# Kernel optimization log

Hardware: AMD Instinct MI355X
Metric: run time of the kernel (lower is better)

## Reference

```python
import jax, jax.numpy as jnp
import numpy as np

N_NODES = 100000
N_EDGES = 600000
N_GRAPHS = 64
DIM_IN = 128


def setup_inputs() -> dict:
    key = jax.random.key(0)
    ks = jax.random.split(key, 12)
    s = 0.05
    return {
        "feat": jax.random.normal(ks[0], (N_NODES, DIM_IN), jnp.float32),
        "Wself1": jax.random.normal(ks[1], (DIM_IN, 100), jnp.float32) * s,
        "Wneigh1": jax.random.normal(ks[2], (DIM_IN, 100), jnp.float32) * s,
        "b1": jnp.zeros((100,), jnp.float32),
        "Wself2": jax.random.normal(ks[3], (100, 20), jnp.float32) * s,
        "Wneigh2": jax.random.normal(ks[4], (100, 20), jnp.float32) * s,
        "b2": jnp.zeros((20,), jnp.float32),
        "fc1_w": jax.random.normal(ks[5], (20, 10), jnp.float32) * s,
        "fc1_b": jnp.zeros((10,), jnp.float32),
        "fc2_w": jax.random.normal(ks[6], (10, 1), jnp.float32) * s,
        "fc2_b": jnp.zeros((1,), jnp.float32),
        "src": jax.random.randint(ks[7], (N_EDGES,), 0, N_NODES, jnp.int32),
        "dst": jax.random.randint(ks[8], (N_EDGES,), 0, N_NODES, jnp.int32),
        "graph_ids": jnp.sort(jax.random.randint(ks[9], (N_NODES,), 0, N_GRAPHS, jnp.int32)),
    }


def _sage_mean(x, src, dst, inv_deg, Wself, Wneigh, b):
    # DGL SAGEConv(aggr='mean'): fc_self(h) + fc_neigh(mean of in-neighbor feats)
    msg = x[src]  # [E, d] gather
    agg = jax.ops.segment_sum(msg, dst, num_segments=N_NODES) * inv_deg  # [N, d]
    return x @ Wself + agg @ Wneigh + b


def reference(feat, Wself1, Wneigh1, b1, Wself2, Wneigh2, b2,
              fc1_w, fc1_b, fc2_w, fc2_b, src, dst, graph_ids):
    ones_e = jnp.ones((src.shape[0],), feat.dtype)
    deg = jax.ops.segment_sum(ones_e, dst, num_segments=N_NODES)
    inv_deg = (1.0 / jnp.maximum(deg, 1.0))[:, None]  # zero in-degree -> agg stays 0

    h = jax.nn.relu(_sage_mean(feat, src, dst, inv_deg, Wself1, Wneigh1, b1))
    h = jax.nn.relu(_sage_mean(h, src, dst, inv_deg, Wself2, Wneigh2, b2))

    # dgl.mean_nodes: per-graph mean over nodes
    ones_n = jnp.ones((h.shape[0],), h.dtype)
    counts = jax.ops.segment_sum(ones_n, graph_ids, num_segments=N_GRAPHS)
    hg = jax.ops.segment_sum(h, graph_ids, num_segments=N_GRAPHS) / jnp.maximum(counts, 1.0)[:, None]

    out = jax.nn.relu(hg @ fc1_w + fc1_b) @ fc2_w + fc2_b  # [G, 1]
    return out
```

## Files before the change

kernel.cpp:

```cpp
#include <hip/hip_runtime.h>
#include <cstddef>

#define N_NODES  100000
#define N_EDGES  600000
#define N_GRAPHS 64

__device__ __forceinline__ void atomAddF(float* p, float v) {
    unsafeAtomicAdd(p, v);
}

__device__ __forceinline__ float f4get(const float4& v, int i) {
    return i == 0 ? v.x : i == 1 ? v.y : i == 2 ? v.z : v.w;
}

typedef __attribute__((address_space(1))) void GV;
typedef __attribute__((address_space(3))) void LV;
__device__ __forceinline__ void gload16(const float* g, float* l) {
    __builtin_amdgcn_global_load_lds((GV*)g, (LV*)l, 16, 0, 0);
}

__global__ __launch_bounds__(256) void deg_count(const int* __restrict__ dst,
                                                 int* __restrict__ deg) {
    int e = blockIdx.x * 256 + threadIdx.x;
    if (e < N_EDGES) atomicAdd(deg + dst[e], 1);
}

__global__ __launch_bounds__(256)
void alloc_ranges(const int* __restrict__ deg, int* __restrict__ beg,
                  int* __restrict__ cur, int* __restrict__ counter) {
    int n = blockIdx.x * 256 + threadIdx.x;
    int d = (n < N_NODES) ? deg[n] : 0;
    int lane = threadIdx.x & 63, wid = threadIdx.x >> 6;
    int incl = d;
#pragma unroll
    for (int o = 1; o < 64; o <<= 1) {
        int v = __shfl_up(incl, o);
        if (lane >= o) incl += v;
    }
    __shared__ int wsum[4];
    __shared__ int blockBase;
    if (lane == 63) wsum[wid] = incl;
    __syncthreads();
    if (threadIdx.x == 0) {
        int tot = wsum[0] + wsum[1] + wsum[2] + wsum[3];
        blockBase = atomicAdd(counter, tot);
    }
    __syncthreads();
    int base = blockBase;
    for (int w = 0; w < wid; ++w) base += wsum[w];
    int start = base + incl - d;
    if (n < N_NODES) { beg[n] = start; cur[n] = start; }
}

__global__ __launch_bounds__(256)
void csr_fill(const int* __restrict__ src, const int* __restrict__ dst,
              int* __restrict__ cur, int* __restrict__ csr_src) {
    int e = blockIdx.x * 256 + threadIdx.x;
    if (e >= N_EDGES) return;
    int p = atomicAdd(cur + dst[e], 1);
    csr_src[p] = src[e];
}

__global__ __launch_bounds__(256, 6)
void gemm1(const float* __restrict__ feat, const float* __restrict__ Wself,
           const float* __restrict__ Wneigh,
           float* __restrict__ S1, float* __restrict__ N1) {
    __shared__ float As[40 * 16];
    __shared__ float Bs[16][200];
    const int tid  = threadIdx.x;
    const int m0   = blockIdx.x * 40;
    const int wave = tid >> 6;
    const int lane = tid & 63;
    const bool active = tid < 250;
    const int tr  = tid / 25;
    const int tcc = tid % 25;
    const int sw  = tr & 3;

    float4 acc0[4], acc1[4];
#pragma unroll
    for (int i = 0; i < 4; ++i) {
        acc0[i] = make_float4(0.f, 0.f, 0.f, 0.f);
        acc1[i] = make_float4(0.f, 0.f, 0.f, 0.f);
    }

    for (int kt = 0; kt < 8; ++kt) {
        const int k0 = kt * 16;
        if (kt) __syncthreads();

        if (lane < 40) {
            int u  = wave * 40 + lane;
            int r  = u >> 2;
            int k4 = (u & 3) ^ ((r >> 2) & 3);
            gload16(feat + (size_t)(m0 + r) * 128 + k0 + k4 * 4, &As[wave * 160]);
        }
        for (int idx = tid; idx < 800; idx += 256) {
            int k = idx / 50, n4 = idx % 50;
            int n = n4 * 4;
            int gk = k0 + k;
            float4 v;
            if (n < 100) v = *reinterpret_cast<const float4*>(Wself + gk * 100 + n);
            else         v = *reinterpret_cast<const float4*>(Wneigh + gk * 100 + (n - 100));
            *reinterpret_cast<float4*>(&Bs[k][n]) = v;
        }
        __syncthreads();

        if (active) {
            const int abase = tr * 64;
#pragma unroll
            for (int g = 0; g < 4; ++g) {
                const int ac = ((g ^ sw) << 2);
                const float4 a0 = *reinterpret_cast<const float4*>(&As[abase +  0 + ac]);
                const float4 a1 = *reinterpret_cast<const float4*>(&As[abase + 16 + ac]);
                const float4 a2 = *reinterpret_cast<const float4*>(&As[abase + 32 + ac]);
                const float4 a3 = *reinterpret_cast<const float4*>(&As[abase + 48 + ac]);
#pragma unroll
                for (int kl = 0; kl < 4; ++kl) {
                    const int k = g * 4 + kl;
                    const float4 b0 = *reinterpret_cast<const float4*>(&Bs[k][tcc * 4]);
                    const float4 b1 = *reinterpret_cast<const float4*>(&Bs[k][100 + tcc * 4]);
                    const float v0 = f4get(a0, kl), v1 = f4get(a1, kl);
                    const float v2 = f4get(a2, kl), v3 = f4get(a3, kl);
                    acc0[0].x = fmaf(v0, b0.x, acc0[0].x); acc0[0].y = fmaf(v0, b0.y, acc0[0].y);
                    acc0[0].z = fmaf(v0, b0.z, acc0[0].z); acc0[0].w = fmaf(v0, b0.w, acc0[0].w);
                    acc1[0].x = fmaf(v0, b1.x, acc1[0].x); acc1[0].y = fmaf(v0, b1.y, acc1[0].y);
                    acc1[0].z = fmaf(v0, b1.z, acc1[0].z); acc1[0].w = fmaf(v0, b1.w, acc1[0].w);
                    acc0[1].x = fmaf(v1, b0.x, acc0[1].x); acc0[1].y = fmaf(v1, b0.y, acc0[1].y);
                    acc0[1].z = fmaf(v1, b0.z, acc0[1].z); acc0[1].w = fmaf(v1, b0.w, acc0[1].w);
                    acc1[1].x = fmaf(v1, b1.x, acc1[1].x); acc1[1].y = fmaf(v1, b1.y, acc1[1].y);
                    acc1[1].z = fmaf(v1, b1.z, acc1[1].z); acc1[1].w = fmaf(v1, b1.w, acc1[1].w);
                    acc0[2].x = fmaf(v2, b0.x, acc0[2].x); acc0[2].y = fmaf(v2, b0.y, acc0[2].y);
                    acc0[2].z = fmaf(v2, b0.z, acc0[2].z); acc0[2].w = fmaf(v2, b0.w, acc0[2].w);
                    acc1[2].x = fmaf(v2, b1.x, acc1[2].x); acc1[2].y = fmaf(v2, b1.y, acc1[2].y);
                    acc1[2].z = fmaf(v2, b1.z, acc1[2].z); acc1[2].w = fmaf(v2, b1.w, acc1[2].w);
                    acc0[3].x = fmaf(v3, b0.x, acc0[3].x); acc0[3].y = fmaf(v3, b0.y, acc0[3].y);
                    acc0[3].z = fmaf(v3, b0.z, acc0[3].z); acc0[3].w = fmaf(v3, b0.w, acc0[3].w);
                    acc1[3].x = fmaf(v3, b1.x, acc1[3].x); acc1[3].y = fmaf(v3, b1.y, acc1[3].y);
                    acc1[3].z = fmaf(v3, b1.z, acc1[3].z); acc1[3].w = fmaf(v3, b1.w, acc1[3].w);
                }
            }
        }
    }

    if (active) {
        const int c = tcc * 4;
#pragma unroll
        for (int i = 0; i < 4; ++i) {
            int gr = m0 + tr * 4 + i;
            *reinterpret_cast<float4*>(S1 + (size_t)gr * 100 + c) = acc0[i];
            *reinterpret_cast<float4*>(N1 + (size_t)gr * 100 + c) = acc1[i];
        }
    }
}

__global__ __launch_bounds__(256)
void aggregate1(const float* __restrict__ N1, const float* __restrict__ S1,
                const float* __restrict__ b1, const int* __restrict__ csr_src,
                const int* __restrict__ beg, const int* __restrict__ cur,
                float* __restrict__ h1) {
    int n  = blockIdx.x * 8 + (threadIdx.x >> 5);
    int c4 = threadIdx.x & 31;
    if (n >= N_NODES || c4 >= 25) return;
    int b = beg[n], end = cur[n];
    float4 acc = make_float4(0.f, 0.f, 0.f, 0.f);
    int j = b;
    for (; j + 1 < end; j += 2) {
        int s0 = csr_src[j], s1 = csr_src[j + 1];
        float4 v0 = *reinterpret_cast<const float4*>(N1 + (size_t)s0 * 100 + c4 * 4);
        float4 v1 = *reinterpret_cast<const float4*>(N1 + (size_t)s1 * 100 + c4 * 4);
        acc.x += v0.x + v1.x; acc.y += v0.y + v1.y;
        acc.z += v0.z + v1.z; acc.w += v0.w + v1.w;
    }
    if (j < end) {
        int s = csr_src[j];
        float4 v = *reinterpret_cast<const float4*>(N1 + (size_t)s * 100 + c4 * 4);
        acc.x += v.x; acc.y += v.y; acc.z += v.z; acc.w += v.w;
    }
    float inv = 1.0f / (float)max(end - b, 1);
    float4 s  = *reinterpret_cast<const float4*>(S1 + (size_t)n * 100 + c4 * 4);
    float4 bb = *reinterpret_cast<const float4*>(b1 + c4 * 4);
    float4 h;
    h.x = fmaxf(fmaf(acc.x, inv, s.x) + bb.x, 0.f);
    h.y = fmaxf(fmaf(acc.y, inv, s.y) + bb.y, 0.f);
    h.z = fmaxf(fmaf(acc.z, inv, s.z) + bb.z, 0.f);
    h.w = fmaxf(fmaf(acc.w, inv, s.w) + bb.w, 0.f);
    *reinterpret_cast<float4*>(h1 + (size_t)n * 100 + c4 * 4) = h;
}

__global__ __launch_bounds__(256)
void gemm2(const float* __restrict__ h1,
           const float* __restrict__ Ws2, const float* __restrict__ Wn2,
           float* __restrict__ S2, float* __restrict__ N2) {
    __shared__ float As[64 * 100];
    __shared__ float Bs[100][40];
    const int tid  = threadIdx.x;
    const int m0   = blockIdx.x * 64;
    const int wave = tid >> 6;
    const int lane = tid & 63;

#pragma unroll
    for (int t = 0; t < 7; ++t) {
        int u0 = t * 256 + wave * 64;
        if (u0 < 1600) {
            int u  = u0 + lane;
            int r  = u / 25, c4 = u % 25;
            int gr = m0 + r; if (gr >= N_NODES) gr = N_NODES - 1;
            gload16(h1 + (size_t)gr * 100 + c4 * 4, &As[u0 * 4]);
        }
    }
    for (int idx = tid; idx < 1000; idx += 256) {
        int k = idx / 10, n4 = idx % 10;
        int n = n4 * 4;
        float4 v;
        if (n < 20) v = *reinterpret_cast<const float4*>(Ws2 + k * 20 + n);
        else        v = *reinterpret_cast<const float4*>(Wn2 + k * 20 + (n - 20));
        *reinterpret_cast<float4*>(&Bs[k][n]) = v;
    }
    __syncthreads();

    const int tr = tid >> 4, tc = tid & 15;
    if (tc < 10) {
        float acc[4][4] = {};
#pragma unroll 4
        for (int k = 0; k < 100; ++k) {
            float a0 = As[(tr * 4 + 0) * 100 + k];
            float a1 = As[(tr * 4 + 1) * 100 + k];
            float a2 = As[(tr * 4 + 2) * 100 + k];
            float a3 = As[(tr * 4 + 3) * 100 + k];
            float4 b = *reinterpret_cast<const float4*>(&Bs[k][tc * 4]);
            acc[0][0] += a0 * b.x; acc[0][1] += a0 * b.y; acc[0][2] += a0 * b.z; acc[0][3] += a0 * b.w;
            acc[1][0] += a1 * b.x; acc[1][1] += a1 * b.y; acc[1][2] += a1 * b.z; acc[1][3] += a1 * b.w;
            acc[2][0] += a2 * b.x; acc[2][1] += a2 * b.y; acc[2][2] += a2 * b.z; acc[2][3] += a2 * b.w;
            acc[3][0] += a3 * b.x; acc[3][1] += a3 * b.y; acc[3][2] += a3 * b.z; acc[3][3] += a3 * b.w;
        }
#pragma unroll
        for (int i = 0; i < 4; ++i) {
            int gr = m0 + tr * 4 + i;
            if (gr >= N_NODES) continue;
            int n = tc * 4;
            float4 v = make_float4(acc[i][0], acc[i][1], acc[i][2], acc[i][3]);
            if (n < 20) *reinterpret_cast<float4*>(S2 + (size_t)gr * 20 + n) = v;
            else        *reinterpret_cast<float4*>(N2 + (size_t)gr * 20 + (n - 20)) = v;
        }
    }
}

__global__ __launch_bounds__(256)
void aggregate2(const float* __restrict__ N2, const float* __restrict__ S2,
                const float* __restrict__ b2, const int* __restrict__ csr_src,
                const int* __restrict__ beg, const int* __restrict__ cur,
                float* __restrict__ h2) {
    int n  = blockIdx.x * 32 + (threadIdx.x >> 3);
    int c4 = threadIdx.x & 7;
    if (n >= N_NODES || c4 >= 5) return;
    int b = beg[n], end = cur[n];
    float4 acc = make_float4(0.f, 0.f, 0.f, 0.f);
    int j = b;
    for (; j + 1 < end; j += 2) {
        int s0 = csr_src[j], s1 = csr_src[j + 1];
        float4 v0 = *reinterpret_cast<const float4*>(N2 + (size_t)s0 * 20 + c4 * 4);
        float4 v1 = *reinterpret_cast<const float4*>(N2 + (size_t)s1 * 20 + c4 * 4);
        acc.x += v0.x + v1.x; acc.y += v0.y + v1.y;
        acc.z += v0.z + v1.z; acc.w += v0.w + v1.w;
    }
    if (j < end) {
        int s = csr_src[j];
        float4 v = *reinterpret_cast<const float4*>(N2 + (size_t)s * 20 + c4 * 4);
        acc.x += v.x; acc.y += v.y; acc.z += v.z; acc.w += v.w;
    }
    float inv = 1.0f / (float)max(end - b, 1);
    float4 s  = *reinterpret_cast<const float4*>(S2 + (size_t)n * 20 + c4 * 4);
    float4 bb = *reinterpret_cast<const float4*>(b2 + c4 * 4);
    float4 h;
    h.x = fmaxf(fmaf(acc.x, inv, s.x) + bb.x, 0.f);
    h.y = fmaxf(fmaf(acc.y, inv, s.y) + bb.y, 0.f);
    h.z = fmaxf(fmaf(acc.z, inv, s.z) + bb.z, 0.f);
    h.w = fmaxf(fmaf(acc.w, inv, s.w) + bb.w, 0.f);
    *reinterpret_cast<float4*>(h2 + (size_t)n * 20 + c4 * 4) = h;
}

__global__ __launch_bounds__(256)
void pool_kernel(const float* __restrict__ h2, const int* __restrict__ gids,
                 float* __restrict__ pool, float* __restrict__ cnt) {
    int n = blockIdx.x * 256 + threadIdx.x;
    float h[20];
    int g = -1;
    if (n < N_NODES) {
        g = gids[n];
#pragma unroll
        for (int q = 0; q < 5; ++q) {
            float4 v = *reinterpret_cast<const float4*>(h2 + (size_t)n * 20 + q * 4);
            h[q * 4 + 0] = v.x; h[q * 4 + 1] = v.y;
            h[q * 4 + 2] = v.z; h[q * 4 + 3] = v.w;
        }
    } else {
#pragma unroll
        for (int c = 0; c < 20; ++c) h[c] = 0.f;
    }
    unsigned long long act = __ballot(n < N_NODES);
    int gfirst = __shfl(g, 0);
    bool uniform = __all(g == gfirst);
    if (uniform) {
        if (gfirst >= 0) {
#pragma unroll
            for (int c = 0; c < 20; ++c)
                for (int off2 = 32; off2 > 0; off2 >>= 1)
                    h[c] += __shfl_down(h[c], off2);
            if ((threadIdx.x & 63) == 0) {
                for (int c = 0; c < 20; ++c) atomAddF(&pool[gfirst * 20 + c], h[c]);
                atomAddF(&cnt[gfirst], (float)__popcll(act));
            }
        }
    } else if (n < N_NODES) {
        for (int c = 0; c < 20; ++c) atomAddF(&pool[g * 20 + c], h[c]);
        atomAddF(&cnt[g], 1.0f);
    }
}

__global__ __launch_bounds__(64)
void head(const float* __restrict__ pool, const float* __restrict__ cnt,
          const float* __restrict__ fc1w, const float* __restrict__ fc1b,
          const float* __restrict__ fc2w, const float* __restrict__ fc2b,
          float* __restrict__ out) {
    int g = threadIdx.x;
    if (g >= N_GRAPHS) return;
    float inv = 1.0f / fmaxf(cnt[g], 1.0f);
    float hg[20];
    for (int c = 0; c < 20; ++c) hg[c] = pool[g * 20 + c] * inv;
    float o = fc2b[0];
    for (int j = 0; j < 10; ++j) {
        float t = fc1b[j];
        for (int c = 0; c < 20; ++c) t = fmaf(hg[c], fc1w[c * 10 + j], t);
        o = fmaf(fmaxf(t, 0.f), fc2w[j], o);
    }
    out[g] = o;
}

extern "C" void kernel_launch(void* const* d_in, const int* in_sizes, int n_in,
                              void* d_out, int out_size, void* d_ws, size_t ws_size,
                              hipStream_t stream) {
    const float* feat   = (const float*)d_in[0];
    const float* Wself1 = (const float*)d_in[1];
    const float* Wneigh1= (const float*)d_in[2];
    const float* b1     = (const float*)d_in[3];
    const float* Wself2 = (const float*)d_in[4];
    const float* Wneigh2= (const float*)d_in[5];
    const float* b2     = (const float*)d_in[6];
    const float* fc1w   = (const float*)d_in[7];
    const float* fc1b   = (const float*)d_in[8];
    const float* fc2w   = (const float*)d_in[9];
    const float* fc2b   = (const float*)d_in[10];
    const int*   src    = (const int*)d_in[11];
    const int*   dst    = (const int*)d_in[12];
    const int*   gids   = (const int*)d_in[13];
    float* ws = (float*)d_ws;

    float* S1 = ws;
    float* N1 = ws + 10000000;
    float* h1 = ws + 20000000;
    float* S2 = N1;
    float* N2 = N1 + 2000000;
    float* h2 = S1;
    int*   deg  = (int*)(ws + 30000000);
    float* pool = ws + 30100000;
    float* cnt  = ws + 30101280;
    int*   ctr  = (int*)(ws + 30101344);
    int*   beg  = (int*)(ws + 30101360);
    int*   cur  = (int*)(ws + 30201360);
    int*   csr  = (int*)(ws + 30301360);

    hipMemsetAsync(deg, 0, (100000 + 1280 + 64 + 16) * sizeof(float), stream);

    deg_count<<<(N_EDGES + 255) / 256, 256, 0, stream>>>(dst, deg);
    alloc_ranges<<<(N_NODES + 255) / 256, 256, 0, stream>>>(deg, beg, cur, ctr);
    csr_fill<<<(N_EDGES + 255) / 256, 256, 0, stream>>>(src, dst, cur, csr);

    gemm1<<<N_NODES / 40, 256, 0, stream>>>(feat, Wself1, Wneigh1, S1, N1);

    aggregate1<<<(N_NODES + 7) / 8, 256, 0, stream>>>(N1, S1, b1, csr, beg, cur, h1);

    gemm2<<<(N_NODES + 63) / 64, 256, 0, stream>>>(h1, Wself2, Wneigh2, S2, N2);

    aggregate2<<<(N_NODES + 31) / 32, 256, 0, stream>>>(N2, S2, b2, csr, beg, cur, h2);

    pool_kernel<<<(N_NODES + 255) / 256, 256, 0, stream>>>(h2, gids, pool, cnt);

    head<<<1, 64, 0, stream>>>(pool, cnt, fc1w, fc1b, fc2w, fc2b, (float*)d_out);
}
```

Before: 296.3 us.

## Double-buffer gemm1 shared tiles and unroll neighbor gathers by four

gemm1 now double-buffers its A and B shared-memory tiles. The next k-tile is prefetched through async LDS loads for A and register staging for B while the current tile is computed, which removes one barrier per iteration and overlaps global loads with FMAs. The cost is twice the LDS and more registers, so the occupancy hint drops from 6 to 5. Both aggregation kernels also gain a 4-way unrolled gather loop so more independent loads are in flight per thread.

```diff
diff --git a/kernel.cpp b/kernel.cpp
--- a/kernel.cpp
+++ b/kernel.cpp
@@ -61,12 +61,21 @@
     csr_src[p] = src[e];
 }
 
-__global__ __launch_bounds__(256, 6)
+__device__ __forceinline__ float4 loadB1(const float* __restrict__ Ws,
+                                         const float* __restrict__ Wn,
+                                         int idx, int k0) {
+    int k = idx / 50, n = (idx % 50) * 4;
+    int gk = k0 + k;
+    return (n < 100) ? *reinterpret_cast<const float4*>(Ws + gk * 100 + n)
+                     : *reinterpret_cast<const float4*>(Wn + gk * 100 + (n - 100));
+}
+
+__global__ __launch_bounds__(256, 5)
 void gemm1(const float* __restrict__ feat, const float* __restrict__ Wself,
            const float* __restrict__ Wneigh,
            float* __restrict__ S1, float* __restrict__ N1) {
-    __shared__ float As[40 * 16];
-    __shared__ float Bs[16][200];
+    __shared__ float As[2][40 * 16];
+    __shared__ float Bs[2][16][200];
     const int tid  = threadIdx.x;
     const int m0   = blockIdx.x * 40;
     const int wave = tid >> 6;
@@ -75,6 +84,10 @@
     const int tr  = tid / 25;
     const int tcc = tid % 25;
     const int sw  = tr & 3;
+    const int bk0 = tid / 50,          bn0 = (tid % 50) * 4;
+    const int bk1 = (tid + 256) / 50,  bn1 = ((tid + 256) % 50) * 4;
+    const int bk2 = (tid + 512) / 50,  bn2 = ((tid + 512) % 50) * 4;
+    const int bk3 = (tid + 768) / 50,  bn3 = ((tid + 768) % 50) * 4;
 
     float4 acc0[4], acc1[4];
 #pragma unroll
@@ -83,41 +96,58 @@
         acc1[i] = make_float4(0.f, 0.f, 0.f, 0.f);
     }
 
+    if (lane < 40) {
+        int u  = wave * 40 + lane;
+        int r  = u >> 2;
+        int k4 = (u & 3) ^ ((r >> 2) & 3);
+        gload16(feat + (size_t)(m0 + r) * 128 + k4 * 4, &As[0][wave * 160]);
+    }
+    {
+        float4 v0 = loadB1(Wself, Wneigh, tid,       0);
+        float4 v1 = loadB1(Wself, Wneigh, tid + 256, 0);
+        float4 v2 = loadB1(Wself, Wneigh, tid + 512, 0);
+        *reinterpret_cast<float4*>(&Bs[0][bk0][bn0]) = v0;
+        *reinterpret_cast<float4*>(&Bs[0][bk1][bn1]) = v1;
+        *reinterpret_cast<float4*>(&Bs[0][bk2][bn2]) = v2;
+        if (tid < 32) {
+            float4 v3 = loadB1(Wself, Wneigh, tid + 768, 0);
+            *reinterpret_cast<float4*>(&Bs[0][bk3][bn3]) = v3;
+        }
+    }
+    __syncthreads();
+
     for (int kt = 0; kt < 8; ++kt) {
-        const int k0 = kt * 16;
-        if (kt) __syncthreads();
-
-        if (lane < 40) {
-            int u  = wave * 40 + lane;
-            int r  = u >> 2;
-            int k4 = (u & 3) ^ ((r >> 2) & 3);
-            gload16(feat + (size_t)(m0 + r) * 128 + k0 + k4 * 4, &As[wave * 160]);
-        }
-        for (int idx = tid; idx < 800; idx += 256) {
-            int k = idx / 50, n4 = idx % 50;
-            int n = n4 * 4;
-            int gk = k0 + k;
-            float4 v;
-            if (n < 100) v = *reinterpret_cast<const float4*>(Wself + gk * 100 + n);
-            else         v = *reinterpret_cast<const float4*>(Wneigh + gk * 100 + (n - 100));
-            *reinterpret_cast<float4*>(&Bs[k][n]) = v;
-        }
-        __syncthreads();
+        const int cb = kt & 1, nb = cb ^ 1;
+        const bool pf = (kt < 7);
+        float4 bv0, bv1, bv2, bv3;
+        if (pf) {
+            const int k0n = (kt + 1) * 16;
+            if (lane < 40) {
+                int u  = wave * 40 + lane;
+                int r  = u >> 2;
+                int k4 = (u & 3) ^ ((r >> 2) & 3);
+                gload16(feat + (size_t)(m0 + r) * 128 + k0n + k4 * 4, &As[nb][wave * 160]);
+            }
+            bv0 = loadB1(Wself, Wneigh, tid,       k0n);
+            bv1 = loadB1(Wself, Wneigh, tid + 256, k0n);
+            bv2 = loadB1(Wself, Wneigh, tid + 512, k0n);
+            if (tid < 32) bv3 = loadB1(Wself, Wneigh, tid + 768, k0n);
+        }
 
         if (active) {
             const int abase = tr * 64;
 #pragma unroll
             for (int g = 0; g < 4; ++g) {
                 const int ac = ((g ^ sw) << 2);
-                const float4 a0 = *reinterpret_cast<const float4*>(&As[abase +  0 + ac]);
-                const float4 a1 = *reinterpret_cast<const float4*>(&As[abase + 16 + ac]);
-                const float4 a2 = *reinterpret_cast<const float4*>(&As[abase + 32 + ac]);
-                const float4 a3 = *reinterpret_cast<const float4*>(&As[abase + 48 + ac]);
+                const float4 a0 = *reinterpret_cast<const float4*>(&As[cb][abase +  0 + ac]);
+                const float4 a1 = *reinterpret_cast<const float4*>(&As[cb][abase + 16 + ac]);
+                const float4 a2 = *reinterpret_cast<const float4*>(&As[cb][abase + 32 + ac]);
+                const float4 a3 = *reinterpret_cast<const float4*>(&As[cb][abase + 48 + ac]);
 #pragma unroll
                 for (int kl = 0; kl < 4; ++kl) {
                     const int k = g * 4 + kl;
-                    const float4 b0 = *reinterpret_cast<const float4*>(&Bs[k][tcc * 4]);
-                    const float4 b1 = *reinterpret_cast<const float4*>(&Bs[k][100 + tcc * 4]);
+                    const float4 b0 = *reinterpret_cast<const float4*>(&Bs[cb][k][tcc * 4]);
+                    const float4 b1 = *reinterpret_cast<const float4*>(&Bs[cb][k][100 + tcc * 4]);
                     const float v0 = f4get(a0, kl), v1 = f4get(a1, kl);
                     const float v2 = f4get(a2, kl), v3 = f4get(a3, kl);
                     acc0[0].x = fmaf(v0, b0.x, acc0[0].x); acc0[0].y = fmaf(v0, b0.y, acc0[0].y);
@@ -139,6 +169,15 @@
                 }
             }
         }
+
+        if (pf) {
+            *reinterpret_cast<float4*>(&Bs[nb][bk0][bn0]) = bv0;
+            *reinterpret_cast<float4*>(&Bs[nb][bk1][bn1]) = bv1;
+            *reinterpret_cast<float4*>(&Bs[nb][bk2][bn2]) = bv2;
+            if (tid < 32)
+                *reinterpret_cast<float4*>(&Bs[nb][bk3][bn3]) = bv3;
+        }
+        __syncthreads();
     }
 
     if (active) {
@@ -163,6 +202,17 @@
     int b = beg[n], end = cur[n];
     float4 acc = make_float4(0.f, 0.f, 0.f, 0.f);
     int j = b;
+    for (; j + 3 < end; j += 4) {
+        int s0 = csr_src[j], s1 = csr_src[j + 1], s2 = csr_src[j + 2], s3 = csr_src[j + 3];
+        float4 v0 = *reinterpret_cast<const float4*>(N1 + (size_t)s0 * 100 + c4 * 4);
+        float4 v1 = *reinterpret_cast<const float4*>(N1 + (size_t)s1 * 100 + c4 * 4);
+        float4 v2 = *reinterpret_cast<const float4*>(N1 + (size_t)s2 * 100 + c4 * 4);
+        float4 v3 = *reinterpret_cast<const float4*>(N1 + (size_t)s3 * 100 + c4 * 4);
+        acc.x += v0.x + v1.x; acc.y += v0.y + v1.y;
+        acc.z += v0.z + v1.z; acc.w += v0.w + v1.w;
+        acc.x += v2.x + v3.x; acc.y += v2.y + v3.y;
+        acc.z += v2.z + v3.z; acc.w += v2.w + v3.w;
+    }
     for (; j + 1 < end; j += 2) {
         int s0 = csr_src[j], s1 = csr_src[j + 1];
         float4 v0 = *reinterpret_cast<const float4*>(N1 + (size_t)s0 * 100 + c4 * 4);
@@ -255,6 +305,17 @@
     int b = beg[n], end = cur[n];
     float4 acc = make_float4(0.f, 0.f, 0.f, 0.f);
     int j = b;
+    for (; j + 3 < end; j += 4) {
+        int s0 = csr_src[j], s1 = csr_src[j + 1], s2 = csr_src[j + 2], s3 = csr_src[j + 3];
+        float4 v0 = *reinterpret_cast<const float4*>(N2 + (size_t)s0 * 20 + c4 * 4);
+        float4 v1 = *reinterpret_cast<const float4*>(N2 + (size_t)s1 * 20 + c4 * 4);
+        float4 v2 = *reinterpret_cast<const float4*>(N2 + (size_t)s2 * 20 + c4 * 4);
+        float4 v3 = *reinterpret_cast<const float4*>(N2 + (size_t)s3 * 20 + c4 * 4);
+        acc.x += v0.x + v1.x; acc.y += v0.y + v1.y;
+        acc.z += v0.z + v1.z; acc.w += v0.w + v1.w;
+        acc.x += v2.x + v3.x; acc.y += v2.y + v3.y;
+        acc.z += v2.z + v3.z; acc.w += v2.w + v3.w;
+    }
     for (; j + 1 < end; j += 2) {
         int s0 = csr_src[j], s1 = csr_src[j + 1];
         float4 v0 = *reinterpret_cast<const float4*>(N2 + (size_t)s0 * 20 + c4 * 4);
```

After: 398.6 us. +34.5%, slower.

## Fuse layer-1 aggregation with layer-2 GEMM and unroll neighbor gathers by four

Applied to the files above, without the earlier changes.

Merges aggregate1 and gemm2 into one kernel. Each block computes h1 for 8 nodes into shared memory and immediately multiplies it by the stacked layer-2 weights, so the h1 intermediate (100k x 100 floats) is never written to or re-read from global memory. The neighbor-gather loops in both aggregation kernels are unrolled by four to keep more loads in flight. In exchange, every block reloads the full 100x40 weight tile into shared memory for only 8 nodes. The small GEMM also uses a simple one-output-per-thread loop, with only 320 of 256x2 thread slots doing work.

```diff
diff --git a/kernel.cpp b/kernel.cpp
--- a/kernel.cpp
+++ b/kernel.cpp
@@ -153,94 +153,75 @@
 }
 
 __global__ __launch_bounds__(256)
-void aggregate1(const float* __restrict__ N1, const float* __restrict__ S1,
+void agg1_gemm2(const float* __restrict__ N1, const float* __restrict__ S1,
                 const float* __restrict__ b1, const int* __restrict__ csr_src,
                 const int* __restrict__ beg, const int* __restrict__ cur,
-                float* __restrict__ h1) {
-    int n  = blockIdx.x * 8 + (threadIdx.x >> 5);
-    int c4 = threadIdx.x & 31;
-    if (n >= N_NODES || c4 >= 25) return;
-    int b = beg[n], end = cur[n];
-    float4 acc = make_float4(0.f, 0.f, 0.f, 0.f);
-    int j = b;
-    for (; j + 1 < end; j += 2) {
-        int s0 = csr_src[j], s1 = csr_src[j + 1];
-        float4 v0 = *reinterpret_cast<const float4*>(N1 + (size_t)s0 * 100 + c4 * 4);
-        float4 v1 = *reinterpret_cast<const float4*>(N1 + (size_t)s1 * 100 + c4 * 4);
-        acc.x += v0.x + v1.x; acc.y += v0.y + v1.y;
-        acc.z += v0.z + v1.z; acc.w += v0.w + v1.w;
-    }
-    if (j < end) {
-        int s = csr_src[j];
-        float4 v = *reinterpret_cast<const float4*>(N1 + (size_t)s * 100 + c4 * 4);
-        acc.x += v.x; acc.y += v.y; acc.z += v.z; acc.w += v.w;
-    }
-    float inv = 1.0f / (float)max(end - b, 1);
-    float4 s  = *reinterpret_cast<const float4*>(S1 + (size_t)n * 100 + c4 * 4);
-    float4 bb = *reinterpret_cast<const float4*>(b1 + c4 * 4);
-    float4 h;
-    h.x = fmaxf(fmaf(acc.x, inv, s.x) + bb.x, 0.f);
-    h.y = fmaxf(fmaf(acc.y, inv, s.y) + bb.y, 0.f);
-    h.z = fmaxf(fmaf(acc.z, inv, s.z) + bb.z, 0.f);
-    h.w = fmaxf(fmaf(acc.w, inv, s.w) + bb.w, 0.f);
-    *reinterpret_cast<float4*>(h1 + (size_t)n * 100 + c4 * 4) = h;
-}
-
-__global__ __launch_bounds__(256)
-void gemm2(const float* __restrict__ h1,
-           const float* __restrict__ Ws2, const float* __restrict__ Wn2,
-           float* __restrict__ S2, float* __restrict__ N2) {
-    __shared__ float As[64 * 100];
-    __shared__ float Bs[100][40];
+                const float* __restrict__ Ws2, const float* __restrict__ Wn2,
+                float* __restrict__ S2, float* __restrict__ N2) {
+    __shared__ float Hs[8][104];
+    __shared__ float Bs2[100][40];
     const int tid  = threadIdx.x;
-    const int m0   = blockIdx.x * 64;
-    const int wave = tid >> 6;
-    const int lane = tid & 63;
-
-#pragma unroll
-    for (int t = 0; t < 7; ++t) {
-        int u0 = t * 256 + wave * 64;
-        if (u0 < 1600) {
-            int u  = u0 + lane;
-            int r  = u / 25, c4 = u % 25;
-            int gr = m0 + r; if (gr >= N_NODES) gr = N_NODES - 1;
-            gload16(h1 + (size_t)gr * 100 + c4 * 4, &As[u0 * 4]);
-        }
-    }
+    const int nloc = tid >> 5;
+    const int c4   = tid & 31;
+    const int n    = blockIdx.x * 8 + nloc;
+
     for (int idx = tid; idx < 1000; idx += 256) {
-        int k = idx / 10, n4 = idx % 10;
-        int n = n4 * 4;
+        int k = idx / 10;
+        int col = (idx % 10) * 4;
         float4 v;
-        if (n < 20) v = *reinterpret_cast<const float4*>(Ws2 + k * 20 + n);
-        else        v = *reinterpret_cast<const float4*>(Wn2 + k * 20 + (n - 20));
-        *reinterpret_cast<float4*>(&Bs[k][n]) = v;
+        if (col < 20) v = *reinterpret_cast<const float4*>(Ws2 + k * 20 + col);
+        else          v = *reinterpret_cast<const float4*>(Wn2 + k * 20 + (col - 20));
+        *reinterpret_cast<float4*>(&Bs2[k][col]) = v;
+    }
+
+    if (c4 < 25) {
+        int b = beg[n], end = cur[n];
+        float4 acc = make_float4(0.f, 0.f, 0.f, 0.f);
+        int j = b;
+        for (; j + 3 < end; j += 4) {
+            int s0 = csr_src[j], s1 = csr_src[j + 1], s2 = csr_src[j + 2], s3 = csr_src[j + 3];
+            float4 v0 = *reinterpret_cast<const float4*>(N1 + (size_t)s0 * 100 + c4 * 4);
+            float4 v1 = *reinterpret_cast<const float4*>(N1 + (size_t)s1 * 100 + c4 * 4);
+            float4 v2 = *reinterpret_cast<const float4*>(N1 + (size_t)s2 * 100 + c4 * 4);
+            float4 v3 = *reinterpret_cast<const float4*>(N1 + (size_t)s3 * 100 + c4 * 4);
+            acc.x += v0.x + v1.x; acc.y += v0.y + v1.y;
+            acc.z += v0.z + v1.z; acc.w += v0.w + v1.w;
+            acc.x += v2.x + v3.x; acc.y += v2.y + v3.y;
+            acc.z += v2.z + v3.z; acc.w += v2.w + v3.w;
+        }
+        for (; j + 1 < end; j += 2) {
+            int s0 = csr_src[j], s1 = csr_src[j + 1];
+            float4 v0 = *reinterpret_cast<const float4*>(N1 + (size_t)s0 * 100 + c4 * 4);
+            float4 v1 = *reinterpret_cast<const float4*>(N1 + (size_t)s1 * 100 + c4 * 4);
+            acc.x += v0.x + v1.x; acc.y += v0.y + v1.y;
+            acc.z += v0.z + v1.z; acc.w += v0.w + v1.w;
+        }
+        if (j < end) {
+            int s = csr_src[j];
+            float4 v = *reinterpret_cast<const float4*>(N1 + (size_t)s * 100 + c4 * 4);
+            acc.x += v.x; acc.y += v.y; acc.z += v.z; acc.w += v.w;
+        }
+        float inv = 1.0f / (float)max(end - b, 1);
+        float4 s  = *reinterpret_cast<const float4*>(S1 + (size_t)n * 100 + c4 * 4);
+        float4 bb = *reinterpret_cast<const float4*>(b1 + c4 * 4);
+        float4 h;
+        h.x = fmaxf(fmaf(acc.x, inv, s.x) + bb.x, 0.f);
+        h.y = fmaxf(fmaf(acc.y, inv, s.y) + bb.y, 0.f);
+        h.z = fmaxf(fmaf(acc.z, inv, s.z) + bb.z, 0.f);
+        h.w = fmaxf(fmaf(acc.w, inv, s.w) + bb.w, 0.f);
+        *reinterpret_cast<float4*>(&Hs[nloc][c4 * 4]) = h;
     }
     __syncthreads();
 
-    const int tr = tid >> 4, tc = tid & 15;
-    if (tc < 10) {
-        float acc[4][4] = {};
+    for (int idx = tid; idx < 320; idx += 256) {
+        int nl = idx / 40, col = idx % 40;
+        float a = 0.f;
 #pragma unroll 4
-        for (int k = 0; k < 100; ++k) {
-            float a0 = As[(tr * 4 + 0) * 100 + k];
-            float a1 = As[(tr * 4 + 1) * 100 + k];
-            float a2 = As[(tr * 4 + 2) * 100 + k];
-            float a3 = As[(tr * 4 + 3) * 100 + k];
-            float4 b = *reinterpret_cast<const float4*>(&Bs[k][tc * 4]);
-            acc[0][0] += a0 * b.x; acc[0][1] += a0 * b.y; acc[0][2] += a0 * b.z; acc[0][3] += a0 * b.w;
-            acc[1][0] += a1 * b.x; acc[1][1] += a1 * b.y; acc[1][2] += a1 * b.z; acc[1][3] += a1 * b.w;
-            acc[2][0] += a2 * b.x; acc[2][1] += a2 * b.y; acc[2][2] += a2 * b.z; acc[2][3] += a2 * b.w;
-            acc[3][0] += a3 * b.x; acc[3][1] += a3 * b.y; acc[3][2] += a3 * b.z; acc[3][3] += a3 * b.w;
-        }
-#pragma unroll
-        for (int i = 0; i < 4; ++i) {
-            int gr = m0 + tr * 4 + i;
-            if (gr >= N_NODES) continue;
-            int n = tc * 4;
-            float4 v = make_float4(acc[i][0], acc[i][1], acc[i][2], acc[i][3]);
-            if (n < 20) *reinterpret_cast<float4*>(S2 + (size_t)gr * 20 + n) = v;
-            else        *reinterpret_cast<float4*>(N2 + (size_t)gr * 20 + (n - 20)) = v;
-        }
+        for (int k = 0; k < 100; ++k)
+            a = fmaf(Hs[nl][k], Bs2[k][col], a);
+        int gn = blockIdx.x * 8 + nl;
+        if (col < 20) S2[(size_t)gn * 20 + col] = a;
+        else          N2[(size_t)gn * 20 + (col - 20)] = a;
     }
 }
 
@@ -255,6 +236,17 @@
     int b = beg[n], end = cur[n];
     float4 acc = make_float4(0.f, 0.f, 0.f, 0.f);
     int j = b;
+    for (; j + 3 < end; j += 4) {
+        int s0 = csr_src[j], s1 = csr_src[j + 1], s2 = csr_src[j + 2], s3 = csr_src[j + 3];
+        float4 v0 = *reinterpret_cast<const float4*>(N2 + (size_t)s0 * 20 + c4 * 4);
+        float4 v1 = *reinterpret_cast<const float4*>(N2 + (size_t)s1 * 20 + c4 * 4);
+        float4 v2 = *reinterpret_cast<const float4*>(N2 + (size_t)s2 * 20 + c4 * 4);
+        float4 v3 = *reinterpret_cast<const float4*>(N2 + (size_t)s3 * 20 + c4 * 4);
+        acc.x += v0.x + v1.x; acc.y += v0.y + v1.y;
+        acc.z += v0.z + v1.z; acc.w += v0.w + v1.w;
+        acc.x += v2.x + v3.x; acc.y += v2.y + v3.y;
+        acc.z += v2.z + v3.z; acc.w += v2.w + v3.w;
+    }
     for (; j + 1 < end; j += 2) {
         int s0 = csr_src[j], s1 = csr_src[j + 1];
         float4 v0 = *reinterpret_cast<const float4*>(N2 + (size_t)s0 * 20 + c4 * 4);
@@ -356,10 +348,9 @@
 
     float* S1 = ws;
     float* N1 = ws + 10000000;
-    float* h1 = ws + 20000000;
-    float* S2 = N1;
-    float* N2 = N1 + 2000000;
-    float* h2 = S1;
+    float* S2 = ws + 20000000;
+    float* N2 = ws + 22000000;
+    float* h2 = ws;
     int*   deg  = (int*)(ws + 30000000);
     float* pool = ws + 30100000;
     float* cnt  = ws + 30101280;
@@ -376,9 +367,8 @@
 
     gemm1<<<N_NODES / 40, 256, 0, stream>>>(feat, Wself1, Wneigh1, S1, N1);
 
-    aggregate1<<<(N_NODES + 7) / 8, 256, 0, stream>>>(N1, S1, b1, csr, beg, cur, h1);
-
-    gemm2<<<(N_NODES + 63) / 64, 256, 0, stream>>>(h1, Wself2, Wneigh2, S2, N2);
+    agg1_gemm2<<<N_NODES / 8, 256, 0, stream>>>(N1, S1, b1, csr, beg, cur,
+                                                Wself2, Wneigh2, S2, N2);
 
     aggregate2<<<(N_NODES + 31) / 32, 256, 0, stream>>>(N2, S2, b2, csr, beg, cur, h2);
 
```

Result: faster. 288.8 us (median of 2 runs) (-2.5%).
